# Performance work log

Hardware: AMD Instinct MI355X
Metric: run time of the kernel (lower is better)

The kernel has to match this reference:

```python
import jax, jax.numpy as jnp
import numpy as np

CODEBOOK_SIZE = 1024
CODEWORD_SIZE = 256
BETA = 0.2  # encoder_fit_vq_factor


def setup_inputs() -> dict:
    key = jax.random.key(0)
    kx, ke = jax.random.split(key)
    x = jax.random.normal(kx, (32, 4096, CODEWORD_SIZE), dtype=jnp.float32)
    # nn.Parameter initialized uniform(-1/n**2, 1/n**2) with n=1 -> U(-1, 1)
    embedding = jax.random.uniform(ke, (CODEBOOK_SIZE, CODEWORD_SIZE),
                                   dtype=jnp.float32, minval=-1.0, maxval=1.0)
    return {"x": x, "embedding": embedding}


def reference(x, embedding):
    x2 = jnp.sum(x * x, axis=-1, keepdims=True)              # [B, N, 1]
    e2 = jnp.sum(embedding * embedding, axis=1)              # [K]
    dist = x2 + e2 - 2.0 * jnp.einsum('bnd,kd->bnk', x, embedding)  # [B, N, K]
    indexes = jnp.argmin(dist, axis=-1)                      # [B, N] int
    # one_hot @ embedding == direct gather
    values = embedding[indexes]                              # [B, N, D]

    loss1 = jnp.mean((jax.lax.stop_gradient(x) - values) ** 2)
    loss2 = jnp.mean((x - jax.lax.stop_gradient(values)) ** 2)
    loss = loss1 + loss2 * BETA

    # straight-through estimator
    values_st = x + jax.lax.stop_gradient(values - x)

    # usage counts (sum of one-hot over all vectors) == scatter-add of ones
    flat_idx = indexes.reshape(-1)
    usages = jnp.zeros((CODEBOOK_SIZE,), dtype=jnp.float32).at[flat_idx].add(1.0)

    return values_st, indexes, loss, usages
```

## Files before the change

kernel.cpp:

```cpp
#include <hip/hip_runtime.h>
#include <cstdint>


#define D 256
#define NCW 1024
#define CHUNK 32
#define NCHUNK 32
#define NK 16
#define TAU 0.00390625f
#define FCAP 8192

typedef _Float16 f16x8 __attribute__((ext_vector_type(8)));
typedef float f32x16 __attribute__((ext_vector_type(16)));
typedef unsigned int u32;
typedef const u32 __attribute__((address_space(1)))* as1_u32p;
typedef u32 __attribute__((address_space(3)))* as3_u32p;

__device__ __forceinline__ void gl_lds16(const void* g, void* s) {
  __builtin_amdgcn_global_load_lds((as1_u32p)(uintptr_t)g,
                                   (as3_u32p)(uint32_t)(uintptr_t)s, 16, 0, 0);
}

__global__ __launch_bounds__(256) void vq_prep(const float* __restrict__ emb,
                                               _Float16* __restrict__ ehf,
                                               _Float16* __restrict__ elf,
                                               float* __restrict__ e2) {
  const int w = threadIdx.x >> 6, l = threadIdx.x & 63;
  const int cw = blockIdx.x * 4 + w;
  const float4 v4 = *(const float4*)(emb + (size_t)cw * D + l * 4);
  const float vv[4] = {v4.x, v4.y, v4.z, v4.w};
  const int chunk = cw >> 5, col = cw & 31;
  double s = 0.0;
#pragma unroll
  for (int i = 0; i < 4; ++i) {
    float v = vv[i];
    s += (double)v * (double)v;
    _Float16 h = (_Float16)v;
    float r = v - (float)h;
    _Float16 lo = (_Float16)(r * 4096.0f);
    int k = l * 4 + i;
    int kk = k >> 4, sub = k & 15;
    int fl = col + ((sub >> 3) << 5);
    int j = sub & 7;
    size_t off = ((size_t)chunk * NK + kk) * 512 + (size_t)fl * 8 + j;
    ehf[off] = h;
    elf[off] = lo;
  }
#pragma unroll
  for (int sft = 1; sft < 64; sft <<= 1) s += __shfl_xor(s, sft);
  if (l == 0) e2[cw] = (float)s;
}

__global__ __launch_bounds__(256, 2) void vq_main(
    const float* __restrict__ x, const float* __restrict__ emb,
    const _Float16* __restrict__ ehf, const _Float16* __restrict__ elf,
    const float* __restrict__ e2g,
    float* __restrict__ out_val, float* __restrict__ out_idx,
    float* __restrict__ out_loss, float* __restrict__ out_usage,
    int* __restrict__ flag_cnt, int2* __restrict__ flags) {
  __shared__ _Float16 eb[2][2][NK][512];
  __shared__ float e2s[NCW];
  __shared__ int idx_s[128];

  const int t = threadIdx.x;
  const int w = t >> 6, l = t & 63;
  const int lc = l & 31, lh = l >> 5;
  const int row0 = blockIdx.x * 128 + w * 32;

  *(float4*)&e2s[t * 4] = *(const float4*)&e2g[t * 4];

  f16x8 xh[NK], xl[NK];
  float x2p = 0.f;
  const float* xp = x + (size_t)(row0 + lc) * D + lh * 8;
#pragma unroll
  for (int kk = 0; kk < NK; ++kk) {
    float4 a = *(const float4*)(xp + kk * 16);
    float4 b = *(const float4*)(xp + kk * 16 + 4);
    float va[8] = {a.x, a.y, a.z, a.w, b.x, b.y, b.z, b.w};
#pragma unroll
    for (int i = 0; i < 8; ++i) {
      float v = va[i];
      _Float16 h = (_Float16)v;
      float r = v - (float)h;
      xh[kk][i] = h;
      xl[kk][i] = (_Float16)(r * 4096.0f);
      x2p = fmaf(v, v, x2p);
    }
  }

  auto stage = [&](int c, int b) {
#pragma unroll
    for (int rr = 0; rr < 4; ++rr) {
      int kk = rr * 4 + w;
      size_t goff = ((size_t)c * NK + kk) * 512 + (size_t)l * 8;
      gl_lds16(ehf + goff, &eb[b][0][kk][0]);
      gl_lds16(elf + goff, &eb[b][1][kk][0]);
    }
  };

  stage(0, 0);
  __syncthreads();

  float minv[16], mini[16], minv2[16];
#pragma unroll
  for (int r = 0; r < 16; ++r) { minv[r] = 3.4e38f; mini[r] = 0.f; minv2[r] = 3.4e38f; }

  for (int c = 0; c < NCHUNK; ++c) {
    const int buf = c & 1;
    if (c + 1 < NCHUNK) stage(c + 1, buf ^ 1);
    const float e2v = e2s[c * CHUNK + lc];

    f32x16 accA, accB;
#pragma unroll
    for (int r = 0; r < 16; ++r) { accA[r] = 0.f; accB[r] = 0.f; }
#pragma unroll
    for (int kk = 0; kk < NK; ++kk) {
      f16x8 bh = *(const f16x8*)&eb[buf][0][kk][l * 8];
      f16x8 bl = *(const f16x8*)&eb[buf][1][kk][l * 8];
      accA = __builtin_amdgcn_mfma_f32_32x32x16_f16(xh[kk], bh, accA, 0, 0, 0);
      accB = __builtin_amdgcn_mfma_f32_32x32x16_f16(xh[kk], bl, accB, 0, 0, 0);
      accB = __builtin_amdgcn_mfma_f32_32x32x16_f16(xl[kk], bh, accB, 0, 0, 0);
    }
    const float colf = (float)(c * CHUNK + lc);
#pragma unroll
    for (int r = 0; r < 16; ++r) {
      float dot = fmaf(accB[r], (1.0f / 4096.0f), accA[r]);
      float tt = fmaf(-2.0f, dot, e2v);
      bool b1 = tt < minv[r];
      float nm2 = b1 ? minv[r] : fminf(tt, minv2[r]);
      minv2[r] = nm2;
      minv[r] = b1 ? tt : minv[r];
      mini[r] = b1 ? colf : mini[r];
    }
    __syncthreads();
  }

#pragma unroll
  for (int s = 1; s < 32; s <<= 1) {
#pragma unroll
    for (int r = 0; r < 16; ++r) {
      float v2 = __shfl_xor(minv[r], s);
      float i2 = __shfl_xor(mini[r], s);
      float w2 = __shfl_xor(minv2[r], s);
      float nm2 = fminf(fminf(minv2[r], w2), fmaxf(minv[r], v2));
      bool take = (v2 < minv[r]) || (v2 == minv[r] && i2 < mini[r]);
      minv[r] = take ? v2 : minv[r];
      mini[r] = take ? i2 : mini[r];
      minv2[r] = nm2;
    }
  }
  const int r = lc;
  const int reg = (r & 3) | ((r >> 3) << 2);
  const int hneed = (r >> 2) & 1;
  float mv = minv[reg], mi = mini[reg], m2 = minv2[reg];
  float mvx = __shfl_xor(mv, 32), mix = __shfl_xor(mi, 32), m2x = __shfl_xor(m2, 32);
  if (hneed != lh) { mv = mvx; mi = mix; m2 = m2x; }
  const float x2row = x2p + __shfl_xor(x2p, 32);

  float lossp = (l < 32) ? (x2row + mv) : 0.f;
#pragma unroll
  for (int s = 1; s < 64; s <<= 1) lossp += __shfl_xor(lossp, s);

  const int idx = (int)mi;
  if (l < 32) {
    out_idx[row0 + r] = mi;
    atomicAdd(&out_usage[idx], 1.0f);
    idx_s[w * 32 + r] = idx;
    if (m2 - mv < TAU) {
      int pos = atomicAdd(flag_cnt, 1);
      if (pos < FCAP) flags[pos] = make_int2(row0 + r, idx);
    }
  }
  if (l == 0) atomicAdd(out_loss, lossp * (1.2f / 33554432.0f));
  __syncthreads();

#pragma unroll 4
  for (int rr = 0; rr < 32; ++rr) {
    int id = idx_s[w * 32 + rr];
    float4 v = *(const float4*)(emb + (size_t)id * D + l * 4);
    *(float4*)(out_val + (size_t)(row0 + rr) * D + l * 4) = v;
  }
}

__global__ __launch_bounds__(256) void vq_refine(
    const float* __restrict__ x, const float* __restrict__ emb,
    const int* __restrict__ flag_cnt, const int2* __restrict__ flags,
    float* __restrict__ out_val, float* __restrict__ out_idx,
    float* __restrict__ out_usage) {
  __shared__ float xs[D];
  __shared__ double bd[256];
  __shared__ int bi[256];
  const int t = threadIdx.x;
  const int cnt = min(*flag_cnt, FCAP);
  for (int f = blockIdx.x; f < cnt; f += gridDim.x) {
    __syncthreads();
    const int row = flags[f].x, old_idx = flags[f].y;
    xs[t] = x[(size_t)row * D + t];
    __syncthreads();
    double best = 1.0e300; int bk = 0;
#pragma unroll
    for (int s = 0; s < 4; ++s) {
      const int k = t + s * 256;
      const float* ep = emb + (size_t)k * D;
      double a0 = 0.0, a1 = 0.0;
      for (int d = 0; d < D; d += 2) {
        double d0 = (double)xs[d] - (double)ep[d];
        double d1 = (double)xs[d + 1] - (double)ep[d + 1];
        a0 = fma(d0, d0, a0);
        a1 = fma(d1, d1, a1);
      }
      double acc = a0 + a1;
      if (acc < best || (acc == best && k < bk)) { best = acc; bk = k; }
    }
    bd[t] = best; bi[t] = bk;
    __syncthreads();
    if (t == 0) {
      double b = bd[0]; int k = bi[0];
      for (int i = 1; i < 256; ++i)
        if (bd[i] < b || (bd[i] == b && bi[i] < k)) { b = bd[i]; k = bi[i]; }
      bi[0] = k;
    }
    __syncthreads();
    const int nk = bi[0];
    if (t == 0 && nk != old_idx) {
      out_idx[row] = (float)nk;
      atomicAdd(&out_usage[old_idx], -1.0f);
      atomicAdd(&out_usage[nk], 1.0f);
    }
    out_val[(size_t)row * D + t] = emb[(size_t)nk * D + t];
  }
}

extern "C" void kernel_launch(void* const* d_in, const int* in_sizes, int n_in,
                              void* d_out, int out_size, void* d_ws, size_t ws_size,
                              hipStream_t stream) {
  (void)n_in; (void)out_size; (void)ws_size;
  const float* x = (const float*)d_in[0];
  const float* emb = (const float*)d_in[1];

  const int n_xelem = in_sizes[0];
  const int n_rows = n_xelem / D;

  float* out = (float*)d_out;
  float* out_val = out;
  float* out_idx = out + n_xelem;
  float* out_loss = out_idx + n_rows;
  float* out_usage = out_loss + 1;

  _Float16* ehf = (_Float16*)d_ws;
  _Float16* elf = ehf + (size_t)NCHUNK * NK * 512;
  float* e2 = (float*)(elf + (size_t)NCHUNK * NK * 512);
  int* flag_cnt = (int*)(e2 + NCW);
  int2* flags = (int2*)(flag_cnt + 2);

  hipMemsetAsync(out_loss, 0, (1 + NCW) * sizeof(float), stream);
  hipMemsetAsync(flag_cnt, 0, sizeof(int), stream);

  vq_prep<<<dim3(NCW / 4), dim3(256), 0, stream>>>(emb, ehf, elf, e2);
  vq_main<<<dim3(n_rows / 128), dim3(256), 0, stream>>>(
      x, emb, ehf, elf, e2, out_val, out_idx, out_loss, out_usage,
      flag_cnt, flags);
  vq_refine<<<dim3(512), dim3(256), 0, stream>>>(
      x, emb, flag_cnt, flags, out_val, out_idx, out_usage);
}
```

Baseline: 501.9 us.

## Drop fp16 hi/lo split in distance GEMM and widen refinement margin

The three-MFMA hi/lo fp16 compensated product becomes a single fp16 MFMA per k-step, split across two accumulators. This removes the low-part codebook staging, its LDS buffer and the e2 LDS copy, and raises the occupancy hint to 3 blocks. The near-tie threshold TAU grows so that rows whose top-two distances are close get recomputed exactly in fp64 by the refine kernel. The two memsets are folded into the prep kernel. The risk is more flagged rows, possibly beyond FCAP, and argmin errors wherever fp16 error exceeds the threshold.

```diff
diff --git a/kernel.cpp b/kernel.cpp
--- a/kernel.cpp
+++ b/kernel.cpp
@@ -7,7 +7,7 @@
 #define CHUNK 32
 #define NCHUNK 32
 #define NK 16
-#define TAU 0.00390625f
+#define TAU 0.03f
 #define FCAP 8192
 
 typedef _Float16 f16x8 __attribute__((ext_vector_type(8)));
@@ -23,8 +23,14 @@
 
 __global__ __launch_bounds__(256) void vq_prep(const float* __restrict__ emb,
                                                _Float16* __restrict__ ehf,
-                                               _Float16* __restrict__ elf,
-                                               float* __restrict__ e2) {
+                                               float* __restrict__ e2,
+                                               float* __restrict__ out_loss,
+                                               int* __restrict__ flag_cnt) {
+  if (blockIdx.x == 255) {
+    for (int i = threadIdx.x; i < 1 + NCW; i += 256) out_loss[i] = 0.f;
+  }
+  if (blockIdx.x == 0 && threadIdx.x == 0) *flag_cnt = 0;
+
   const int w = threadIdx.x >> 6, l = threadIdx.x & 63;
   const int cw = blockIdx.x * 4 + w;
   const float4 v4 = *(const float4*)(emb + (size_t)cw * D + l * 4);
@@ -36,30 +42,24 @@
     float v = vv[i];
     s += (double)v * (double)v;
     _Float16 h = (_Float16)v;
-    float r = v - (float)h;
-    _Float16 lo = (_Float16)(r * 4096.0f);
     int k = l * 4 + i;
     int kk = k >> 4, sub = k & 15;
     int fl = col + ((sub >> 3) << 5);
     int j = sub & 7;
-    size_t off = ((size_t)chunk * NK + kk) * 512 + (size_t)fl * 8 + j;
-    ehf[off] = h;
-    elf[off] = lo;
+    ehf[((size_t)chunk * NK + kk) * 512 + (size_t)fl * 8 + j] = h;
   }
 #pragma unroll
   for (int sft = 1; sft < 64; sft <<= 1) s += __shfl_xor(s, sft);
   if (l == 0) e2[cw] = (float)s;
 }
 
-__global__ __launch_bounds__(256, 2) void vq_main(
+__global__ __launch_bounds__(256, 3) void vq_main(
     const float* __restrict__ x, const float* __restrict__ emb,
-    const _Float16* __restrict__ ehf, const _Float16* __restrict__ elf,
-    const float* __restrict__ e2g,
+    const _Float16* __restrict__ ehf, const float* __restrict__ e2g,
     float* __restrict__ out_val, float* __restrict__ out_idx,
     float* __restrict__ out_loss, float* __restrict__ out_usage,
     int* __restrict__ flag_cnt, int2* __restrict__ flags) {
-  __shared__ _Float16 eb[2][2][NK][512];
-  __shared__ float e2s[NCW];
+  __shared__ _Float16 eb[2][NK][512];
   __shared__ int idx_s[128];
 
   const int t = threadIdx.x;
@@ -67,9 +67,7 @@
   const int lc = l & 31, lh = l >> 5;
   const int row0 = blockIdx.x * 128 + w * 32;
 
-  *(float4*)&e2s[t * 4] = *(const float4*)&e2g[t * 4];
-
-  f16x8 xh[NK], xl[NK];
+  f16x8 xh[NK];
   float x2p = 0.f;
   const float* xp = x + (size_t)(row0 + lc) * D + lh * 8;
 #pragma unroll
@@ -80,10 +78,7 @@
 #pragma unroll
     for (int i = 0; i < 8; ++i) {
       float v = va[i];
-      _Float16 h = (_Float16)v;
-      float r = v - (float)h;
-      xh[kk][i] = h;
-      xl[kk][i] = (_Float16)(r * 4096.0f);
+      xh[kk][i] = (_Float16)v;
       x2p = fmaf(v, v, x2p);
     }
   }
@@ -92,9 +87,7 @@
 #pragma unroll
     for (int rr = 0; rr < 4; ++rr) {
       int kk = rr * 4 + w;
-      size_t goff = ((size_t)c * NK + kk) * 512 + (size_t)l * 8;
-      gl_lds16(ehf + goff, &eb[b][0][kk][0]);
-      gl_lds16(elf + goff, &eb[b][1][kk][0]);
+      gl_lds16(ehf + ((size_t)c * NK + kk) * 512 + (size_t)l * 8, &eb[b][kk][0]);
     }
   };
 
@@ -108,29 +101,27 @@
   for (int c = 0; c < NCHUNK; ++c) {
     const int buf = c & 1;
     if (c + 1 < NCHUNK) stage(c + 1, buf ^ 1);
-    const float e2v = e2s[c * CHUNK + lc];
-
-    f32x16 accA, accB;
-#pragma unroll
-    for (int r = 0; r < 16; ++r) { accA[r] = 0.f; accB[r] = 0.f; }
-#pragma unroll
-    for (int kk = 0; kk < NK; ++kk) {
-      f16x8 bh = *(const f16x8*)&eb[buf][0][kk][l * 8];
-      f16x8 bl = *(const f16x8*)&eb[buf][1][kk][l * 8];
-      accA = __builtin_amdgcn_mfma_f32_32x32x16_f16(xh[kk], bh, accA, 0, 0, 0);
-      accB = __builtin_amdgcn_mfma_f32_32x32x16_f16(xh[kk], bl, accB, 0, 0, 0);
-      accB = __builtin_amdgcn_mfma_f32_32x32x16_f16(xl[kk], bh, accB, 0, 0, 0);
+    const float e2v = e2g[c * CHUNK + lc];
+
+    f32x16 accE, accO;
+#pragma unroll
+    for (int r = 0; r < 16; ++r) { accE[r] = 0.f; accO[r] = 0.f; }
+#pragma unroll
+    for (int kk = 0; kk < NK; kk += 2) {
+      f16x8 b0 = *(const f16x8*)&eb[buf][kk][l * 8];
+      f16x8 b1 = *(const f16x8*)&eb[buf][kk + 1][l * 8];
+      accE = __builtin_amdgcn_mfma_f32_32x32x16_f16(xh[kk], b0, accE, 0, 0, 0);
+      accO = __builtin_amdgcn_mfma_f32_32x32x16_f16(xh[kk + 1], b1, accO, 0, 0, 0);
     }
     const float colf = (float)(c * CHUNK + lc);
 #pragma unroll
     for (int r = 0; r < 16; ++r) {
-      float dot = fmaf(accB[r], (1.0f / 4096.0f), accA[r]);
-      float tt = fmaf(-2.0f, dot, e2v);
-      bool b1 = tt < minv[r];
-      float nm2 = b1 ? minv[r] : fminf(tt, minv2[r]);
+      float tt = fmaf(-2.0f, accE[r] + accO[r], e2v);
+      float nm2 = fminf(fmaxf(tt, minv[r]), minv2[r]);
+      bool b1m = tt < minv[r];
       minv2[r] = nm2;
-      minv[r] = b1 ? tt : minv[r];
-      mini[r] = b1 ? colf : mini[r];
+      minv[r] = b1m ? tt : minv[r];
+      mini[r] = b1m ? colf : mini[r];
     }
     __syncthreads();
   }
@@ -248,18 +239,13 @@
   float* out_usage = out_loss + 1;
 
   _Float16* ehf = (_Float16*)d_ws;
-  _Float16* elf = ehf + (size_t)NCHUNK * NK * 512;
-  float* e2 = (float*)(elf + (size_t)NCHUNK * NK * 512);
+  float* e2 = (float*)(ehf + (size_t)NCHUNK * NK * 512);
   int* flag_cnt = (int*)(e2 + NCW);
   int2* flags = (int2*)(flag_cnt + 2);
 
-  hipMemsetAsync(out_loss, 0, (1 + NCW) * sizeof(float), stream);
-  hipMemsetAsync(flag_cnt, 0, sizeof(int), stream);
-
-  vq_prep<<<dim3(NCW / 4), dim3(256), 0, stream>>>(emb, ehf, elf, e2);
+  vq_prep<<<dim3(NCW / 4), dim3(256), 0, stream>>>(emb, ehf, e2, out_loss, flag_cnt);
   vq_main<<<dim3(n_rows / 128), dim3(256), 0, stream>>>(
-      x, emb, ehf, elf, e2, out_val, out_idx, out_loss, out_usage,
-      flag_cnt, flags);
+      x, emb, ehf, e2, out_val, out_idx, out_loss, out_usage, flag_cnt, flags);
   vq_refine<<<dim3(512), dim3(256), 0, stream>>>(
       x, emb, flag_cnt, flags, out_val, out_idx, out_usage);
 }
```

Measured after the change: 744.2 us. 48.3% more time.
